# Kernel tuning notes

Measured on AMD Instinct MI355X. Metric: run time of the kernel, lower is better.

The kernel has to match this reference:

```python
import jax, jax.numpy as jnp
import numpy as np

N, C, D, V, NC = 60000, 4, 200, 5000, 250


def _lin(key, out_d, in_d):
    # torch nn.Linear default init: U(-1/sqrt(in), 1/sqrt(in))
    s = 1.0 / np.sqrt(in_d)
    k1, k2 = jax.random.split(key)
    w = jax.random.uniform(k1, (out_d, in_d), minval=-s, maxval=s, dtype=jnp.float32)
    b = jax.random.uniform(k2, (out_d,), minval=-s, maxval=s, dtype=jnp.float32)
    return w, b


def setup_inputs() -> dict:
    key = jax.random.key(0)
    ks = jax.random.split(key, 16)
    inp = {}
    inp['tokens'] = jax.random.randint(ks[0], (N,), 0, V)
    inp['child_c'] = jax.random.normal(ks[1], (N, C, D), dtype=jnp.float32)
    inp['child_h'] = jax.random.normal(ks[2], (N, C, D), dtype=jnp.float32)
    inp['emb'] = jax.random.normal(ks[3], (V, D), dtype=jnp.float32)
    # ForBlock: proj1: 3D->D, proj2: 2D->D
    inp['p1_w'], inp['p1_b'] = _lin(ks[4], D, 3 * D)
    inp['p2_w'], inp['p2_b'] = _lin(ks[5], D, 2 * D)
    # treelstm gates (each Linear D->D)
    for i, g in enumerate(['ix', 'ih', 'fx', 'fh', 'ux', 'uh', 'ox', 'oh']):
        w, b = _lin(ks[6 + i], D, D)
        inp[g + '_w'], inp[g + '_b'] = w, b
    inp['fc2_w'], inp['fc2_b'] = _lin(ks[14], NC, D)
    return inp


def reference(tokens, child_c, child_h, emb,
              p1_w, p1_b, p2_w, p2_b,
              ix_w, ix_b, ih_w, ih_b, fx_w, fx_b, fh_w, fh_b,
              ux_w, ux_b, uh_w, uh_b, ox_w, ox_b, oh_w, oh_b,
              fc2_w, fc2_b):
    x = emb[tokens]  # [N, D] node token embeddings (nn.Embedding lookup)
    # ForBlock: control = relu(proj1(cat[init, cond, next])); hsum = relu(proj2(cat[control, block]))
    control = jax.nn.relu(
        jnp.concatenate([child_h[:, 0], child_h[:, 1], child_h[:, 2]], axis=-1) @ p1_w.T + p1_b)
    child_h_sum = jax.nn.relu(
        jnp.concatenate([control, child_h[:, 3]], axis=-1) @ p2_w.T + p2_b)  # [N, D]
    # treelstm.node update (vectorized over N nodes, C children)
    i = jax.nn.sigmoid(x @ ix_w.T + ix_b + child_h_sum @ ih_w.T + ih_b)
    o = jax.nn.sigmoid(x @ ox_w.T + ox_b + child_h_sum @ oh_w.T + oh_b)
    u = jnp.tanh(x @ ux_w.T + ux_b + child_h_sum @ uh_w.T + uh_b)
    fx = (x @ fx_w.T + fx_b)[:, None, :]  # [N, 1, D]
    f = jax.nn.sigmoid(jnp.einsum('ncd,md->ncm', child_h, fh_w) + fh_b + fx)  # [N, C, D]
    c = i * u + jnp.sum(f * child_c, axis=1)  # [N, D]
    h = o * jnp.tanh(c)  # [N, D]
    logits = h @ fc2_w.T + fc2_b  # [N, n_class]
    return logits
```

## Files before the change

### kernel.cpp

```cpp
#include <hip/hip_runtime.h>
#include <cmath>

#define NNODES 60000
#define DDIM   200
#define NCLS   250

constexpr int R   = 32;
constexpr int BK  = 32;
constexpr int XP  = 208;

constexpr int O_X  = 0;
constexpr int O_H  = R * XP;
constexpr int O_A  = 2 * R * XP;
constexpr int AS   = R * BK;
constexpr int O_W  = O_A + 2 * AS;
constexpr int WS   = 8192;
constexpr int SH_TOT = O_W + 2 * WS + 32;

typedef float  f32x4  __attribute__((ext_vector_type(4)));
typedef short  short8 __attribute__((ext_vector_type(8)));

constexpr int W_P1  = 0;
constexpr int W_P2A = 155648;
constexpr int W_P2B = 212992;
constexpr int W_FX  = 270336;
constexpr int W_FH  = 327680;
constexpr int W_IX  = 385024;
constexpr int W_IH  = 442368;
constexpr int W_UX  = 499712;
constexpr int W_UH  = 557056;
constexpr int W_OX  = 614400;
constexpr int W_OH  = 671744;
constexpr int W_FC2 = 729088;
constexpr int W_TOTAL_ELEMS = 786432;
constexpr size_t W_TOTAL_BYTES = (size_t)W_TOTAL_ELEMS * 2;

__device__ __forceinline__ short f2b(float f) {
    union { float f; unsigned u; } x; x.f = f;
    unsigned r = (x.u + 0x7FFFu + ((x.u >> 16) & 1u)) >> 16;
    return (short)r;
}
__device__ __forceinline__ unsigned cvtpk(float lo, float hi) {
    unsigned r; asm("v_cvt_pk_bf16_f32 %0, %1, %2" : "=v"(r) : "v"(lo), "v"(hi));
    return r;
}
__device__ __forceinline__ short f2b1(float f) { return (short)(cvtpk(f, f) & 0xffffu); }
__device__ __forceinline__ float b2f(short s) {
    union { unsigned u; float f; } x; x.u = ((unsigned)(unsigned short)s) << 16;
    return x.f;
}
__device__ __forceinline__ float b2f_lo(unsigned u) { return b2f((short)(u & 0xffffu)); }
__device__ __forceinline__ float b2f_hi(unsigned u) { return b2f((short)(u >> 16)); }
__device__ __forceinline__ float sgm(float x)  { return 1.0f / (1.0f + __expf(-x)); }
__device__ __forceinline__ float tanh_fast(float x) { return 1.0f - 2.0f / (__expf(2.0f * x) + 1.0f); }
__device__ __forceinline__ int   swz(int b)    { return b ^ (((b >> 7) & 3) << 4); }
__device__ __forceinline__ short8 cvt8(float4 f0, float4 f1) {
    union { unsigned u[4]; short8 s; } c;
    c.u[0] = cvtpk(f0.x, f0.y); c.u[1] = cvtpk(f0.z, f0.w);
    c.u[2] = cvtpk(f1.x, f1.y); c.u[3] = cvtpk(f1.z, f1.w);
    return c.s;
}

__global__ void wprep(const float* __restrict__ p1w, const float* __restrict__ p2w,
                      const float* __restrict__ fxw, const float* __restrict__ fhw,
                      const float* __restrict__ ixw, const float* __restrict__ ihw,
                      const float* __restrict__ uxw, const float* __restrict__ uhw,
                      const float* __restrict__ oxw, const float* __restrict__ ohw,
                      const float* __restrict__ fc2w, short* __restrict__ ws)
{
    int i = blockIdx.x * 256 + threadIdx.x;
    if (i >= W_TOTAL_ELEMS) return;
    float v = 0.0f;
    if (i < W_P2A) {
        int n = i / 608, k = i % 608;
        if (n < 200 && k < 600) v = p1w[n * 600 + k];
        ws[i] = f2b(v); return;
    }
    int j = i - W_P2A;
    int m = j / 57344, rem = j % 57344;
    int n = rem / 224, k = rem % 224;
    const float* src; int stride = 200, off = 0, ncols = 200;
    switch (m) {
        case 0:  src = p2w; stride = 400; break;
        case 1:  src = p2w; stride = 400; off = 200; break;
        case 2:  src = fxw; break;
        case 3:  src = fhw; break;
        case 4:  src = ixw; break;
        case 5:  src = ihw; break;
        case 6:  src = uxw; break;
        case 7:  src = uhw; break;
        case 8:  src = oxw; break;
        case 9:  src = ohw; break;
        default: src = fc2w; ncols = 250; break;
    }
    if (n < ncols && k < 200) v = src[n * stride + off + k];
    ws[i] = f2b(v);
}

__device__ __forceinline__ void gload16(const void* g, void* l) {
    __builtin_amdgcn_global_load_lds((const __attribute__((address_space(1))) unsigned*)g,
                                     (__attribute__((address_space(3))) unsigned*)l, 16, 0, 0);
}

__device__ __forceinline__ void stage_w(const short* __restrict__ wmat, int Kpad, int t,
                                        int wrows, int wv, short* w_sw)
{
    const int issues = wrows >> 4;
    for (int q = wv; q < issues; q += 4) {
        const int lane = threadIdx.x & 63;
        const int db = q * 1024 + lane * 16;
        const int n  = db >> 6;
        const int g  = (db >> 4) & 3;
        const int gs = g ^ ((n >> 1) & 3);
        const short* src = wmat + (long)n * Kpad + t * BK + gs * 8;
        char* dst = ((char*)w_sw) + q * 1024;
        gload16(src, dst);
    }
}

__device__ __forceinline__ void stage_a_chh(short* a_sw, const float* __restrict__ ag,
                                            int row0, int colofs, int k0, int Kreal, int tid)
{
    if (tid >= 4 * R) return;
    const int r = tid >> 2, gq = tid & 3;
    const float* src = ag + (long)(row0 + r) * 800 + colofs + k0 + gq * 8;
    short8 v;
    if (k0 + BK <= Kreal) {
        float4 f0 = *(const float4*)(src);
        float4 f1 = *(const float4*)(src + 4);
        v = cvt8(f0, f1);
    } else {
        #pragma unroll
        for (int i = 0; i < 8; ++i) {
            int k = k0 + gq * 8 + i;
            float f = (k < Kreal) ? src[i] : 0.0f;
            v[i] = f2b(f);
        }
    }
    int b = r * 64 + gq * 16; b = swz(b);
    *(short8*)((char*)a_sw + b) = v;
}

template<int NF, bool FROM_GLOBAL>
__device__ __forceinline__ void gemm_pass(
    f32x4 (&acc)[NF],
    const short* __restrict__ Ap,
    const float* __restrict__ ag, int row0, int colofs, int Kreal,
    const short* __restrict__ wmat, int ktiles, int Kpad, int wrows,
    short* a_sw, short* w_sw,
    int tid, int wv, int wm, int wn, int l15, int lg)
{
    stage_w(wmat, Kpad, 0, wrows, wv, w_sw);
    if constexpr (FROM_GLOBAL)
        stage_a_chh(a_sw, ag, row0, colofs, 0, Kreal, tid);
    asm volatile("s_waitcnt vmcnt(0) lgkmcnt(0)" ::: "memory");
    __builtin_amdgcn_s_barrier();
    for (int t = 0; t < ktiles; ++t) {
        const int cur = t & 1, nxt = cur ^ 1;
        if (t + 1 < ktiles) {
            stage_w(wmat, Kpad, t + 1, wrows, wv, w_sw + nxt * WS);
            if constexpr (FROM_GLOBAL)
                stage_a_chh(a_sw + nxt * AS, ag, row0, colofs, (t + 1) * BK, Kreal, tid);
        }
        short8 af;
        const int row = wm * 16 + l15;
        if constexpr (FROM_GLOBAL)
            af = *(const short8*)((const char*)(a_sw + cur * AS) + swz(row * 64 + lg * 16));
        else
            af = *(const short8*)(Ap + row * XP + t * BK + lg * 8);
        #pragma unroll
        for (int ni = 0; ni < NF; ++ni) {
            const int n = (wn * NF + ni) * 16 + l15;
            short8 bf = *(const short8*)((const char*)(w_sw + cur * WS) + swz(n * 64 + lg * 16));
            acc[ni] = __builtin_amdgcn_mfma_f32_16x16x32_bf16(af, bf, acc[ni], 0, 0, 0);
        }
        asm volatile("s_waitcnt vmcnt(0) lgkmcnt(0)" ::: "memory");
        __builtin_amdgcn_s_barrier();
    }
}

#define Z7(A)  { _Pragma("unroll") for (int z_=0; z_<7; ++z_) { _Pragma("unroll") for (int q_=0;q_<4;++q_) A[z_][q_] = 0.0f; } }
#define Z8(A)  { _Pragma("unroll") for (int z_=0; z_<8; ++z_) { _Pragma("unroll") for (int q_=0;q_<4;++q_) A[z_][q_] = 0.0f; } }

__global__ __launch_bounds__(256, 2)
void fused_v7(const int* __restrict__ tok,
              const float* __restrict__ chc,
              const float* __restrict__ chh,
              const float* __restrict__ emb,
              const float* __restrict__ p1b_, const float* __restrict__ p2b_,
              const float* __restrict__ ixb, const float* __restrict__ ihb,
              const float* __restrict__ fxb, const float* __restrict__ fhb,
              const float* __restrict__ uxb, const float* __restrict__ uhb,
              const float* __restrict__ oxb, const float* __restrict__ ohb,
              const float* __restrict__ fc2b,
              const short* __restrict__ ws,
              float* __restrict__ out)
{
    __shared__ __align__(16) short SH[SH_TOT];
    short* X    = SH + O_X;
    short* H    = SH + O_H;
    short* a_sw = SH + O_A;
    short* w_sw = SH + O_W;

    const int tid = threadIdx.x;
    const int wv = tid >> 6, wm = wv >> 1, wn = wv & 1;
    const int l15 = tid & 15, lg = (tid & 63) >> 4;
    const int row0 = blockIdx.x * R;

    {
        short8 z = (short8)0;
        short8* shv = (short8*)SH;
        #pragma unroll 1
        for (int i = tid; i < SH_TOT / 8; i += 256) shv[i] = z;
    }
    __syncthreads();
    {
        #pragma unroll
        for (int it = 0; it < 4; ++it) {
            int u = tid + it * 256;
            if (u < 800) {
                int r = u / 25, cu = (u % 25) * 8;
                const float* s = emb + (long)tok[row0 + r] * DDIM + cu;
                float4 f0 = *(const float4*)s, f1 = *(const float4*)(s + 4);
                *(short8*)(X + r * XP + cu) = cvt8(f0, f1);
            }
        }
    }
    __syncthreads();

    f32x4 g[7];

    unsigned fxr[7][2];
    Z7(g);
    gemm_pass<7, false>(g, X, nullptr, 0, 0, 0, ws + W_FX, 7, 224, 224,
                        a_sw, w_sw, tid, wv, wm, wn, l15, lg);
    #pragma unroll
    for (int ni = 0; ni < 7; ++ni) {
        const int col = (wn * 7 + ni) * 16 + l15;
        const float b = (col < DDIM) ? fxb[col] : 0.0f;
        fxr[ni][0] = cvtpk(g[ni][0] + b, g[ni][1] + b);
        fxr[ni][1] = cvtpk(g[ni][2] + b, g[ni][3] + b);
    }

    float csum[7][4];
    #pragma unroll
    for (int ni = 0; ni < 7; ++ni)
        #pragma unroll
        for (int j = 0; j < 4; ++j) csum[ni][j] = 0.0f;

    #pragma unroll 1
    for (int c = 0; c < 4; ++c) {
        Z7(g);
        gemm_pass<7, true>(g, nullptr, chh, row0, c * 200, 200, ws + W_FH, 7, 224, 224,
                           a_sw, w_sw, tid, wv, wm, wn, l15, lg);
        #pragma unroll
        for (int ni = 0; ni < 7; ++ni) {
            const int col = (wn * 7 + ni) * 16 + l15;
            if (col < DDIM) {
                const float fb = fhb[col];
                #pragma unroll
                for (int j = 0; j < 4; ++j) {
                    const int lr = wm * 16 + lg * 4 + j;
                    const float cv = chc[(long)(row0 + lr) * 800 + c * 200 + col];
                    const unsigned pk = fxr[ni][j >> 1];
                    const float fx = (j & 1) ? b2f_hi(pk) : b2f_lo(pk);
                    csum[ni][j] += sgm(g[ni][j] + fb + fx) * cv;
                }
            }
        }
    }

    Z7(g);
    gemm_pass<7, true>(g, nullptr, chh, row0, 0, 600, ws + W_P1, 19, 608, 224,
                       a_sw, w_sw, tid, wv, wm, wn, l15, lg);
    #pragma unroll
    for (int ni = 0; ni < 7; ++ni) {
        const int col = (wn * 7 + ni) * 16 + l15;
        if (col < DDIM) {
            const float b = p1b_[col];
            #pragma unroll
            for (int j = 0; j < 4; ++j) {
                const int lr = wm * 16 + lg * 4 + j;
                H[lr * XP + col] = f2b1(fmaxf(g[ni][j] + b, 0.0f));
            }
        }
    }
    __syncthreads();

    Z7(g);
    gemm_pass<7, false>(g, H, nullptr, 0, 0, 0, ws + W_P2A, 7, 224, 224,
                        a_sw, w_sw, tid, wv, wm, wn, l15, lg);
    gemm_pass<7, true>(g, nullptr, chh, row0, 600, 200, ws + W_P2B, 7, 224, 224,
                       a_sw, w_sw, tid, wv, wm, wn, l15, lg);
    #pragma unroll
    for (int ni = 0; ni < 7; ++ni) {
        const int col = (wn * 7 + ni) * 16 + l15;
        if (col < DDIM) {
            const float b = p2b_[col];
            #pragma unroll
            for (int j = 0; j < 4; ++j) {
                const int lr = wm * 16 + lg * 4 + j;
                H[lr * XP + col] = f2b1(fmaxf(g[ni][j] + b, 0.0f));
            }
        }
    }
    __syncthreads();

    unsigned gi[7][2];
    Z7(g);
    gemm_pass<7, false>(g, X, nullptr, 0, 0, 0, ws + W_IX, 7, 224, 224,
                        a_sw, w_sw, tid, wv, wm, wn, l15, lg);
    gemm_pass<7, false>(g, H, nullptr, 0, 0, 0, ws + W_IH, 7, 224, 224,
                        a_sw, w_sw, tid, wv, wm, wn, l15, lg);
    #pragma unroll
    for (int ni = 0; ni < 7; ++ni) {
        const int col = (wn * 7 + ni) * 16 + l15;
        const float b = (col < DDIM) ? (ixb[col] + ihb[col]) : 0.0f;
        gi[ni][0] = cvtpk(sgm(g[ni][0] + b), sgm(g[ni][1] + b));
        gi[ni][1] = cvtpk(sgm(g[ni][2] + b), sgm(g[ni][3] + b));
    }

    Z7(g);
    gemm_pass<7, false>(g, X, nullptr, 0, 0, 0, ws + W_UX, 7, 224, 224,
                        a_sw, w_sw, tid, wv, wm, wn, l15, lg);
    gemm_pass<7, false>(g, H, nullptr, 0, 0, 0, ws + W_UH, 7, 224, 224,
                        a_sw, w_sw, tid, wv, wm, wn, l15, lg);
    #pragma unroll
    for (int ni = 0; ni < 7; ++ni) {
        const int col = (wn * 7 + ni) * 16 + l15;
        const float b = (col < DDIM) ? (uxb[col] + uhb[col]) : 0.0f;
        #pragma unroll
        for (int j = 0; j < 4; ++j) {
            const unsigned pk = gi[ni][j >> 1];
            const float iv = (j & 1) ? b2f_hi(pk) : b2f_lo(pk);
            csum[ni][j] = iv * tanh_fast(g[ni][j] + b) + csum[ni][j];
        }
    }

    Z7(g);
    gemm_pass<7, false>(g, X, nullptr, 0, 0, 0, ws + W_OX, 7, 224, 224,
                        a_sw, w_sw, tid, wv, wm, wn, l15, lg);
    gemm_pass<7, false>(g, H, nullptr, 0, 0, 0, ws + W_OH, 7, 224, 224,
                        a_sw, w_sw, tid, wv, wm, wn, l15, lg);
    #pragma unroll
    for (int ni = 0; ni < 7; ++ni) {
        const int col = (wn * 7 + ni) * 16 + l15;
        if (col < DDIM) {
            const float b = oxb[col] + ohb[col];
            #pragma unroll
            for (int j = 0; j < 4; ++j) {
                const int lr = wm * 16 + lg * 4 + j;
                H[lr * XP + col] = f2b1(sgm(g[ni][j] + b) * tanh_fast(csum[ni][j]));
            }
        }
    }
    __syncthreads();

    f32x4 o8[8];
    Z8(o8);
    gemm_pass<8, false>(o8, H, nullptr, 0, 0, 0, ws + W_FC2, 7, 224, 256,
                        a_sw, w_sw, tid, wv, wm, wn, l15, lg);
    #pragma unroll
    for (int ni = 0; ni < 8; ++ni) {
        const int col = (wn * 8 + ni) * 16 + l15;
        if (col < NCLS) {
            const float b = fc2b[col];
            #pragma unroll
            for (int j = 0; j < 4; ++j) {
                const int lr = wm * 16 + lg * 4 + j;
                out[(long)(row0 + lr) * NCLS + col] = o8[ni][j] + b;
            }
        }
    }
}

constexpr int FRT = 32, FBK = 16, FNT = 256, FRTP = FRT + 4, FBUFP = 208;
__device__ __forceinline__ float sgm_f(float x) { return 1.0f / (1.0f + expf(-x)); }

__device__ __forceinline__ void f_stage(
    float (*aT)[FRTP], float (*wt)[FNT], int row0, int k0,
    const float* a1g, int a1pitch, const int* gidx, const float* a1l, int a1lp, int K1,
    const float* a2g, int a2pitch, const float* a2l, int a2lp, int K2,
    const float* wa, int wap, int KW1, const float* wb, int wbp,
    int ncols, int tid)
{
    const int Ktot = K1 + K2;
    {
        const int kk = tid & 15, k = k0 + kk;
        #pragma unroll
        for (int h = 0; h < 2; ++h) {
            const int r = (tid >> 4) + h * 16;
            float v = 0.0f;
            if (k < K1) {
                if (a1l) v = a1l[r * a1lp + k];
                else {
                    const long rb = gidx ? (long)gidx[row0 + r] * a1pitch : (long)(row0 + r) * a1pitch;
                    v = a1g[rb + k];
                }
            } else if (k < Ktot) {
                if (a2l) v = a2l[r * a2lp + (k - K1)];
                else     v = a2g[(long)(row0 + r) * a2pitch + (k - K1)];
            }
            aT[kk][r] = v;
        }
    }
    {
        const int col = tid;
        #pragma unroll
        for (int kk = 0; kk < FBK; ++kk) {
            const int k = k0 + kk; float v = 0.0f;
            if (col < ncols && k < Ktot) {
                if (k < KW1) v = wa[(long)col * wap + k];
                else         v = wb[(long)col * wbp + (k - KW1)];
            }
            wt[kk][col] = v;
        }
    }
}
__device__ __forceinline__ void f_gemm(
    float (*aT)[FRTP], float (*wt)[FNT], float acc[8][4], int row0,
    const float* a1g, int a1p, const int* gidx, const float* a1l, int a1lp, int K1,
    const float* a2g, int a2p, const float* a2l, int a2lp, int K2,
    const float* wa, int wap, int KW1, const float* wb, int wbp,
    int ncols, int tid, int tr, int tc)
{
    #pragma unroll
    for (int j = 0; j < 8; ++j)
        #pragma unroll
        for (int i = 0; i < 4; ++i) acc[j][i] = 0.0f;
    const int Ktot = K1 + K2;
    for (int k0 = 0; k0 < Ktot; k0 += FBK) {
        __syncthreads();
        f_stage(aT, wt, row0, k0, a1g, a1p, gidx, a1l, a1lp, K1, a2g, a2p, a2l, a2lp, K2,
                wa, wap, KW1, wb, wbp, ncols, tid);
        __syncthreads();
        #pragma unroll
        for (int kk = 0; kk < FBK; ++kk) {
            const float w0 = wt[kk][tc*4+0], w1 = wt[kk][tc*4+1], w2 = wt[kk][tc*4+2], w3 = wt[kk][tc*4+3];
            #pragma unroll
            for (int j = 0; j < 8; ++j) {
                const float a = aT[kk][tr*8+j];
                acc[j][0] = fmaf(a, w0, acc[j][0]); acc[j][1] = fmaf(a, w1, acc[j][1]);
                acc[j][2] = fmaf(a, w2, acc[j][2]); acc[j][3] = fmaf(a, w3, acc[j][3]);
            }
        }
    }
}
__global__ __launch_bounds__(256)
void fused_fp32(const int* tok, const float* chc, const float* chh, const float* emb,
                const float* p1w, const float* p1b, const float* p2w, const float* p2b,
                const float* ixw, const float* ixb, const float* ihw, const float* ihb,
                const float* fxw, const float* fxb, const float* fhw, const float* fhb,
                const float* uxw, const float* uxb, const float* uhw, const float* uhb,
                const float* oxw, const float* oxb, const float* ohw, const float* ohb,
                const float* fc2w, const float* fc2b, float* out)
{
    __shared__ float aT[FBK][FRTP]; __shared__ float wt[FBK][FNT]; __shared__ float buf[FRT][FBUFP];
    const int tid = threadIdx.x, tr = tid >> 6, tc = tid & 63, c0 = tc * 4;
    const int row0 = blockIdx.x * FRT;
    float acc[8][4];
    f_gemm(aT, wt, acc, row0, chh, 800, nullptr, nullptr, 0, 600, nullptr,0,nullptr,0,0, p1w,600,600,nullptr,0, DDIM, tid,tr,tc);
    if (c0 < DDIM) { const float4 b = *(const float4*)&p1b[c0];
        #pragma unroll
        for (int j=0;j<8;++j){int r=tr*8+j; buf[r][c0]=fmaxf(acc[j][0]+b.x,0.f); buf[r][c0+1]=fmaxf(acc[j][1]+b.y,0.f); buf[r][c0+2]=fmaxf(acc[j][2]+b.z,0.f); buf[r][c0+3]=fmaxf(acc[j][3]+b.w,0.f);} }
    f_gemm(aT, wt, acc, row0, nullptr,0,nullptr,&buf[0][0],FBUFP,200, chh+600,800,nullptr,0,200, p2w,400,400,nullptr,0, DDIM, tid,tr,tc);
    if (c0 < DDIM) { const float4 b = *(const float4*)&p2b[c0];
        #pragma unroll
        for (int j=0;j<8;++j){int r=tr*8+j; buf[r][c0]=fmaxf(acc[j][0]+b.x,0.f); buf[r][c0+1]=fmaxf(acc[j][1]+b.y,0.f); buf[r][c0+2]=fmaxf(acc[j][2]+b.z,0.f); buf[r][c0+3]=fmaxf(acc[j][3]+b.w,0.f);} }
    f_gemm(aT, wt, acc, row0, emb, DDIM, tok, nullptr,0,200, nullptr,0,nullptr,0,0, fxw,200,200,nullptr,0, DDIM, tid,tr,tc);
    float fxr[8][4];
    { float4 b = make_float4(0,0,0,0); if (c0<DDIM) b = *(const float4*)&fxb[c0];
      #pragma unroll
      for (int j=0;j<8;++j){fxr[j][0]=acc[j][0]+b.x;fxr[j][1]=acc[j][1]+b.y;fxr[j][2]=acc[j][2]+b.z;fxr[j][3]=acc[j][3]+b.w;} }
    float csum[8][4];
    #pragma unroll
    for (int j=0;j<8;++j)
        #pragma unroll
        for (int i=0;i<4;++i) csum[j][i]=0.f;
    for (int cc_=0; cc_<4; ++cc_) {
        f_gemm(aT, wt, acc, row0, chh+cc_*200,800,nullptr,nullptr,0,200, nullptr,0,nullptr,0,0, fhw,200,200,nullptr,0, DDIM, tid,tr,tc);
        if (c0 < DDIM) { const float4 b = *(const float4*)&fhb[c0];
            #pragma unroll
            for (int j=0;j<8;++j){ const long r=row0+tr*8+j; const float4 cv=*(const float4*)&chc[r*800+cc_*200+c0];
                csum[j][0]+=sgm_f(acc[j][0]+b.x+fxr[j][0])*cv.x; csum[j][1]+=sgm_f(acc[j][1]+b.y+fxr[j][1])*cv.y;
                csum[j][2]+=sgm_f(acc[j][2]+b.z+fxr[j][2])*cv.z; csum[j][3]+=sgm_f(acc[j][3]+b.w+fxr[j][3])*cv.w; } }
    }
    f_gemm(aT, wt, acc, row0, emb, DDIM, tok, nullptr,0,200, nullptr,0,&buf[0][0],FBUFP,200, ixw,200,200,ihw,200, DDIM, tid,tr,tc);
    float gi[8][4];
    { float4 b1=make_float4(0,0,0,0),b2=b1; if(c0<DDIM){b1=*(const float4*)&ixb[c0];b2=*(const float4*)&ihb[c0];}
      #pragma unroll
      for(int j=0;j<8;++j){gi[j][0]=sgm_f(acc[j][0]+b1.x+b2.x);gi[j][1]=sgm_f(acc[j][1]+b1.y+b2.y);gi[j][2]=sgm_f(acc[j][2]+b1.z+b2.z);gi[j][3]=sgm_f(acc[j][3]+b1.w+b2.w);} }
    f_gemm(aT, wt, acc, row0, emb, DDIM, tok, nullptr,0,200, nullptr,0,&buf[0][0],FBUFP,200, uxw,200,200,uhw,200, DDIM, tid,tr,tc);
    float cval[8][4];
    { float4 b1=make_float4(0,0,0,0),b2=b1; if(c0<DDIM){b1=*(const float4*)&uxb[c0];b2=*(const float4*)&uhb[c0];}
      #pragma unroll
      for(int j=0;j<8;++j){cval[j][0]=gi[j][0]*tanhf(acc[j][0]+b1.x+b2.x)+csum[j][0];cval[j][1]=gi[j][1]*tanhf(acc[j][1]+b1.y+b2.y)+csum[j][1];
                           cval[j][2]=gi[j][2]*tanhf(acc[j][2]+b1.z+b2.z)+csum[j][2];cval[j][3]=gi[j][3]*tanhf(acc[j][3]+b1.w+b2.w)+csum[j][3];} }
    f_gemm(aT, wt, acc, row0, emb, DDIM, tok, nullptr,0,200, nullptr,0,&buf[0][0],FBUFP,200, oxw,200,200,ohw,200, DDIM, tid,tr,tc);
    if (c0 < DDIM) { const float4 b1=*(const float4*)&oxb[c0], b2=*(const float4*)&ohb[c0];
        #pragma unroll
        for(int j=0;j<8;++j){int r=tr*8+j;
            buf[r][c0]=sgm_f(acc[j][0]+b1.x+b2.x)*tanhf(cval[j][0]); buf[r][c0+1]=sgm_f(acc[j][1]+b1.y+b2.y)*tanhf(cval[j][1]);
            buf[r][c0+2]=sgm_f(acc[j][2]+b1.z+b2.z)*tanhf(cval[j][2]); buf[r][c0+3]=sgm_f(acc[j][3]+b1.w+b2.w)*tanhf(cval[j][3]);} }
    f_gemm(aT, wt, acc, row0, nullptr,0,nullptr,&buf[0][0],FBUFP,200, nullptr,0,nullptr,0,0, fc2w,200,200,nullptr,0, NCLS, tid,tr,tc);
    #pragma unroll
    for (int j=0;j<8;++j){ const long r=row0+tr*8+j;
        #pragma unroll
        for (int i=0;i<4;++i){ const int col=c0+i; if (col<NCLS) out[r*NCLS+col]=acc[j][i]+fc2b[col]; } }
}

extern "C" void kernel_launch(void* const* d_in, const int* in_sizes, int n_in,
                              void* d_out, int out_size, void* d_ws, size_t ws_size,
                              hipStream_t stream)
{
    const int*   tok  = (const int*)  d_in[0];
    const float* chc  = (const float*)d_in[1];
    const float* chh  = (const float*)d_in[2];
    const float* emb  = (const float*)d_in[3];
    const float* p1w  = (const float*)d_in[4];
    const float* p1b  = (const float*)d_in[5];
    const float* p2w  = (const float*)d_in[6];
    const float* p2b  = (const float*)d_in[7];
    const float* ixw  = (const float*)d_in[8];
    const float* ixb  = (const float*)d_in[9];
    const float* ihw  = (const float*)d_in[10];
    const float* ihb  = (const float*)d_in[11];
    const float* fxw  = (const float*)d_in[12];
    const float* fxb  = (const float*)d_in[13];
    const float* fhw  = (const float*)d_in[14];
    const float* fhb  = (const float*)d_in[15];
    const float* uxw  = (const float*)d_in[16];
    const float* uxb  = (const float*)d_in[17];
    const float* uhw  = (const float*)d_in[18];
    const float* uhb  = (const float*)d_in[19];
    const float* oxw  = (const float*)d_in[20];
    const float* oxb  = (const float*)d_in[21];
    const float* ohw  = (const float*)d_in[22];
    const float* ohb  = (const float*)d_in[23];
    const float* fc2w = (const float*)d_in[24];
    const float* fc2b = (const float*)d_in[25];
    float* out = (float*)d_out;

    if (ws_size >= W_TOTAL_BYTES) {
        short* ws = (short*)d_ws;
        hipLaunchKernelGGL(wprep, dim3((W_TOTAL_ELEMS + 255) / 256), dim3(256), 0, stream,
                           p1w, p2w, fxw, fhw, ixw, ihw, uxw, uhw, oxw, ohw, fc2w, ws);
        hipLaunchKernelGGL(fused_v7, dim3(NNODES / R), dim3(256), 0, stream,
                           tok, chc, chh, emb,
                           p1b, p2b, ixb, ihb, fxb, fhb, uxb, uhb, oxb, ohb, fc2b,
                           ws, out);
    } else {
        hipLaunchKernelGGL(fused_fp32, dim3(NNODES / FRT), dim3(256), 0, stream,
                           tok, chc, chh, emb, p1w, p1b, p2w, p2b,
                           ixw, ixb, ihw, ihb, fxw, fxb, fhw, fhb,
                           uxw, uxb, uhw, uhb, oxw, oxb, ohw, ohb, fc2w, fc2b, out);
    }
}
```

Before: 449.8 us.

## Double row tile to 64 with 512-thread blocks and restage gate epilogues

Each block now handles 64 rows with 8 waves arranged 2x4, and each wave computes two M sub-tiles against four N sub-tiles, so every staged weight tile feeds twice as many MFMAs. The stage order changes: proj1/proj2 run first, then the i/u/o gates, whose results are kept packed in registers, then the forget-gate loop, which builds the cell state directly. Padding is changed to XP=232 and bounds clamps are added because 60000 is not a multiple of 64. The goal is to cut repeated weight staging and barrier overhead per row. The cost is roughly 100KB of LDS per block, which allows only one block per CU, plus higher register pressure.

Result: slower. 492.1 us (+9.4%).

```diff
diff --git a/kernel.cpp b/kernel.cpp
--- a/kernel.cpp
+++ b/kernel.cpp
@@ -5,9 +5,9 @@
 #define DDIM   200
 #define NCLS   250
 
-constexpr int R   = 32;
+constexpr int R   = 64;
 constexpr int BK  = 32;
-constexpr int XP  = 208;
+constexpr int XP  = 232;
 
 constexpr int O_X  = 0;
 constexpr int O_H  = R * XP;
@@ -106,7 +106,7 @@
                                         int wrows, int wv, short* w_sw)
 {
     const int issues = wrows >> 4;
-    for (int q = wv; q < issues; q += 4) {
+    for (int q = wv; q < issues; q += 8) {
         const int lane = threadIdx.x & 63;
         const int db = q * 1024 + lane * 16;
         const int n  = db >> 6;
@@ -123,7 +123,8 @@
 {
     if (tid >= 4 * R) return;
     const int r = tid >> 2, gq = tid & 3;
-    const float* src = ag + (long)(row0 + r) * 800 + colofs + k0 + gq * 8;
+    long rg = row0 + r; if (rg >= NNODES) rg = NNODES - 1;
+    const float* src = ag + rg * 800 + colofs + k0 + gq * 8;
     short8 v;
     if (k0 + BK <= Kreal) {
         float4 f0 = *(const float4*)(src);
@@ -143,7 +144,7 @@
 
 template<int NF, bool FROM_GLOBAL>
 __device__ __forceinline__ void gemm_pass(
-    f32x4 (&acc)[NF],
+    f32x4 (&acc)[2][NF],
     const short* __restrict__ Ap,
     const float* __restrict__ ag, int row0, int colofs, int Kreal,
     const short* __restrict__ wmat, int ktiles, int Kpad, int wrows,
@@ -153,8 +154,7 @@
     stage_w(wmat, Kpad, 0, wrows, wv, w_sw);
     if constexpr (FROM_GLOBAL)
         stage_a_chh(a_sw, ag, row0, colofs, 0, Kreal, tid);
-    asm volatile("s_waitcnt vmcnt(0) lgkmcnt(0)" ::: "memory");
-    __builtin_amdgcn_s_barrier();
+    __syncthreads();
     for (int t = 0; t < ktiles; ++t) {
         const int cur = t & 1, nxt = cur ^ 1;
         if (t + 1 < ktiles) {
@@ -162,28 +162,30 @@
             if constexpr (FROM_GLOBAL)
                 stage_a_chh(a_sw + nxt * AS, ag, row0, colofs, (t + 1) * BK, Kreal, tid);
         }
-        short8 af;
-        const int row = wm * 16 + l15;
-        if constexpr (FROM_GLOBAL)
-            af = *(const short8*)((const char*)(a_sw + cur * AS) + swz(row * 64 + lg * 16));
-        else
-            af = *(const short8*)(Ap + row * XP + t * BK + lg * 8);
+        short8 af[2];
+        #pragma unroll
+        for (int mi = 0; mi < 2; ++mi) {
+            const int row = wm * 32 + mi * 16 + l15;
+            if constexpr (FROM_GLOBAL)
+                af[mi] = *(const short8*)((const char*)(a_sw + cur * AS) + swz(row * 64 + lg * 16));
+            else
+                af[mi] = *(const short8*)(Ap + row * XP + t * BK + lg * 8);
+        }
         #pragma unroll
         for (int ni = 0; ni < NF; ++ni) {
             const int n = (wn * NF + ni) * 16 + l15;
             short8 bf = *(const short8*)((const char*)(w_sw + cur * WS) + swz(n * 64 + lg * 16));
-            acc[ni] = __builtin_amdgcn_mfma_f32_16x16x32_bf16(af, bf, acc[ni], 0, 0, 0);
-        }
-        asm volatile("s_waitcnt vmcnt(0) lgkmcnt(0)" ::: "memory");
-        __builtin_amdgcn_s_barrier();
-    }
-}
-
-#define Z7(A)  { _Pragma("unroll") for (int z_=0; z_<7; ++z_) { _Pragma("unroll") for (int q_=0;q_<4;++q_) A[z_][q_] = 0.0f; } }
-#define Z8(A)  { _Pragma("unroll") for (int z_=0; z_<8; ++z_) { _Pragma("unroll") for (int q_=0;q_<4;++q_) A[z_][q_] = 0.0f; } }
-
-__global__ __launch_bounds__(256, 2)
-void fused_v7(const int* __restrict__ tok,
+            acc[0][ni] = __builtin_amdgcn_mfma_f32_16x16x32_bf16(af[0], bf, acc[0][ni], 0, 0, 0);
+            acc[1][ni] = __builtin_amdgcn_mfma_f32_16x16x32_bf16(af[1], bf, acc[1][ni], 0, 0, 0);
+        }
+        __syncthreads();
+    }
+}
+
+#define Z24(A)  { _Pragma("unroll") for (int m_=0;m_<2;++m_) { _Pragma("unroll") for (int z_=0; z_<4; ++z_) { _Pragma("unroll") for (int q_=0;q_<4;++q_) A[m_][z_][q_] = 0.0f; } } }
+
+__global__ __launch_bounds__(512, 1)
+void fused_v8(const int* __restrict__ tok,
               const float* __restrict__ chc,
               const float* __restrict__ chh,
               const float* __restrict__ emb,
@@ -203,7 +205,9 @@
     short* w_sw = SH + O_W;
 
     const int tid = threadIdx.x;
-    const int wv = tid >> 6, wm = wv >> 1, wn = wv & 1;
+    const int wv  = tid >> 6;
+    const int wm  = wv >> 2;
+    const int wn  = wv & 3;
     const int l15 = tid & 15, lg = (tid & 63) >> 4;
     const int row0 = blockIdx.x * R;
 
@@ -211,167 +215,195 @@
         short8 z = (short8)0;
         short8* shv = (short8*)SH;
         #pragma unroll 1
-        for (int i = tid; i < SH_TOT / 8; i += 256) shv[i] = z;
+        for (int i = tid; i < SH_TOT / 8; i += 512) shv[i] = z;
     }
     __syncthreads();
     {
-        #pragma unroll
-        for (int it = 0; it < 4; ++it) {
-            int u = tid + it * 256;
-            if (u < 800) {
-                int r = u / 25, cu = (u % 25) * 8;
-                const float* s = emb + (long)tok[row0 + r] * DDIM + cu;
-                float4 f0 = *(const float4*)s, f1 = *(const float4*)(s + 4);
-                *(short8*)(X + r * XP + cu) = cvt8(f0, f1);
-            }
+        #pragma unroll 1
+        for (int u = tid; u < 1600; u += 512) {
+            int r = u / 25, cu = (u % 25) * 8;
+            long rg = row0 + r; if (rg >= NNODES) rg = NNODES - 1;
+            const float* s = emb + (long)tok[rg] * DDIM + cu;
+            float4 f0 = *(const float4*)s, f1 = *(const float4*)(s + 4);
+            *(short8*)(X + r * XP + cu) = cvt8(f0, f1);
         }
     }
     __syncthreads();
 
-    f32x4 g[7];
-
-    unsigned fxr[7][2];
-    Z7(g);
-    gemm_pass<7, false>(g, X, nullptr, 0, 0, 0, ws + W_FX, 7, 224, 224,
-                        a_sw, w_sw, tid, wv, wm, wn, l15, lg);
-    #pragma unroll
-    for (int ni = 0; ni < 7; ++ni) {
-        const int col = (wn * 7 + ni) * 16 + l15;
-        const float b = (col < DDIM) ? fxb[col] : 0.0f;
-        fxr[ni][0] = cvtpk(g[ni][0] + b, g[ni][1] + b);
-        fxr[ni][1] = cvtpk(g[ni][2] + b, g[ni][3] + b);
-    }
-
-    float csum[7][4];
-    #pragma unroll
-    for (int ni = 0; ni < 7; ++ni)
-        #pragma unroll
-        for (int j = 0; j < 4; ++j) csum[ni][j] = 0.0f;
+    f32x4 g[2][4];
+
+    Z24(g);
+    gemm_pass<4, true>(g, nullptr, chh, row0, 0, 600, ws + W_P1, 19, 608, 224,
+                       a_sw, w_sw, tid, wv, wm, wn, l15, lg);
+    #pragma unroll
+    for (int mi = 0; mi < 2; ++mi)
+        #pragma unroll
+        for (int ni = 0; ni < 4; ++ni) {
+            const int col = (wn * 4 + ni) * 16 + l15;
+            if (col < DDIM) {
+                const float b = p1b_[col];
+                #pragma unroll
+                for (int j = 0; j < 4; ++j) {
+                    const int lr = wm * 32 + mi * 16 + lg * 4 + j;
+                    H[lr * XP + col] = f2b1(fmaxf(g[mi][ni][j] + b, 0.0f));
+                }
+            }
+        }
+
+    Z24(g);
+    gemm_pass<4, false>(g, H, nullptr, 0, 0, 0, ws + W_P2A, 7, 224, 224,
+                        a_sw, w_sw, tid, wv, wm, wn, l15, lg);
+    gemm_pass<4, true>(g, nullptr, chh, row0, 600, 200, ws + W_P2B, 7, 224, 224,
+                       a_sw, w_sw, tid, wv, wm, wn, l15, lg);
+    #pragma unroll
+    for (int mi = 0; mi < 2; ++mi)
+        #pragma unroll
+        for (int ni = 0; ni < 4; ++ni) {
+            const int col = (wn * 4 + ni) * 16 + l15;
+            if (col < DDIM) {
+                const float b = p2b_[col];
+                #pragma unroll
+                for (int j = 0; j < 4; ++j) {
+                    const int lr = wm * 32 + mi * 16 + lg * 4 + j;
+                    H[lr * XP + col] = f2b1(fmaxf(g[mi][ni][j] + b, 0.0f));
+                }
+            }
+        }
+
+    unsigned gi[2][4][2];
+    Z24(g);
+    gemm_pass<4, false>(g, X, nullptr, 0, 0, 0, ws + W_IX, 7, 224, 224,
+                        a_sw, w_sw, tid, wv, wm, wn, l15, lg);
+    gemm_pass<4, false>(g, H, nullptr, 0, 0, 0, ws + W_IH, 7, 224, 224,
+                        a_sw, w_sw, tid, wv, wm, wn, l15, lg);
+    #pragma unroll
+    for (int mi = 0; mi < 2; ++mi)
+        #pragma unroll
+        for (int ni = 0; ni < 4; ++ni) {
+            const int col = (wn * 4 + ni) * 16 + l15;
+            const float b = (col < DDIM) ? (ixb[col] + ihb[col]) : 0.0f;
+            gi[mi][ni][0] = cvtpk(sgm(g[mi][ni][0] + b), sgm(g[mi][ni][1] + b));
+            gi[mi][ni][1] = cvtpk(sgm(g[mi][ni][2] + b), sgm(g[mi][ni][3] + b));
+        }
+
+    unsigned iu[2][4][2];
+    Z24(g);
+    gemm_pass<4, false>(g, X, nullptr, 0, 0, 0, ws + W_UX, 7, 224, 224,
+                        a_sw, w_sw, tid, wv, wm, wn, l15, lg);
+    gemm_pass<4, false>(g, H, nullptr, 0, 0, 0, ws + W_UH, 7, 224, 224,
+                        a_sw, w_sw, tid, wv, wm, wn, l15, lg);
+    #pragma unroll
+    for (int mi = 0; mi < 2; ++mi)
+        #pragma unroll
+        for (int ni = 0; ni < 4; ++ni) {
+            const int col = (wn * 4 + ni) * 16 + l15;
+            const float b = (col < DDIM) ? (uxb[col] + uhb[col]) : 0.0f;
+            float v0 = b2f_lo(gi[mi][ni][0]) * tanh_fast(g[mi][ni][0] + b);
+            float v1 = b2f_hi(gi[mi][ni][0]) * tanh_fast(g[mi][ni][1] + b);
+            float v2 = b2f_lo(gi[mi][ni][1]) * tanh_fast(g[mi][ni][2] + b);
+            float v3 = b2f_hi(gi[mi][ni][1]) * tanh_fast(g[mi][ni][3] + b);
+            iu[mi][ni][0] = cvtpk(v0, v1);
+            iu[mi][ni][1] = cvtpk(v2, v3);
+        }
+
+    unsigned og[2][4][2];
+    Z24(g);
+    gemm_pass<4, false>(g, X, nullptr, 0, 0, 0, ws + W_OX, 7, 224, 224,
+                        a_sw, w_sw, tid, wv, wm, wn, l15, lg);
+    gemm_pass<4, false>(g, H, nullptr, 0, 0, 0, ws + W_OH, 7, 224, 224,
+                        a_sw, w_sw, tid, wv, wm, wn, l15, lg);
+    #pragma unroll
+    for (int mi = 0; mi < 2; ++mi)
+        #pragma unroll
+        for (int ni = 0; ni < 4; ++ni) {
+            const int col = (wn * 4 + ni) * 16 + l15;
+            const float b = (col < DDIM) ? (oxb[col] + ohb[col]) : 0.0f;
+            og[mi][ni][0] = cvtpk(sgm(g[mi][ni][0] + b), sgm(g[mi][ni][1] + b));
+            og[mi][ni][1] = cvtpk(sgm(g[mi][ni][2] + b), sgm(g[mi][ni][3] + b));
+        }
+
+    unsigned fxr[2][4][2];
+    Z24(g);
+    gemm_pass<4, false>(g, X, nullptr, 0, 0, 0, ws + W_FX, 7, 224, 224,
+                        a_sw, w_sw, tid, wv, wm, wn, l15, lg);
+    #pragma unroll
+    for (int mi = 0; mi < 2; ++mi)
+        #pragma unroll
+        for (int ni = 0; ni < 4; ++ni) {
+            const int col = (wn * 4 + ni) * 16 + l15;
+            const float b = (col < DDIM) ? fxb[col] : 0.0f;
+            fxr[mi][ni][0] = cvtpk(g[mi][ni][0] + b, g[mi][ni][1] + b);
+            fxr[mi][ni][1] = cvtpk(g[mi][ni][2] + b, g[mi][ni][3] + b);
+        }
+
+    float csum[2][4][4];
+    #pragma unroll
+    for (int mi = 0; mi < 2; ++mi)
+        #pragma unroll
+        for (int ni = 0; ni < 4; ++ni)
+            #pragma unroll
+            for (int j = 0; j < 4; ++j) csum[mi][ni][j] = 0.0f;
 
     #pragma unroll 1
     for (int c = 0; c < 4; ++c) {
-        Z7(g);
-        gemm_pass<7, true>(g, nullptr, chh, row0, c * 200, 200, ws + W_FH, 7, 224, 224,
+        Z24(g);
+        gemm_pass<4, true>(g, nullptr, chh, row0, c * 200, 200, ws + W_FH, 7, 224, 224,
                            a_sw, w_sw, tid, wv, wm, wn, l15, lg);
         #pragma unroll
-        for (int ni = 0; ni < 7; ++ni) {
-            const int col = (wn * 7 + ni) * 16 + l15;
+        for (int mi = 0; mi < 2; ++mi)
+            #pragma unroll
+            for (int ni = 0; ni < 4; ++ni) {
+                const int col = (wn * 4 + ni) * 16 + l15;
+                if (col < DDIM) {
+                    const float fb = fhb[col];
+                    #pragma unroll
+                    for (int j = 0; j < 4; ++j) {
+                        long rg = row0 + wm * 32 + mi * 16 + lg * 4 + j;
+                        if (rg >= NNODES) rg = NNODES - 1;
+                        const float cv = chc[rg * 800 + c * 200 + col];
+                        const unsigned pk = fxr[mi][ni][j >> 1];
+                        const float fx = (j & 1) ? b2f_hi(pk) : b2f_lo(pk);
+                        csum[mi][ni][j] += sgm(g[mi][ni][j] + fb + fx) * cv;
+                    }
+                }
+            }
+    }
+
+    #pragma unroll
+    for (int mi = 0; mi < 2; ++mi)
+        #pragma unroll
+        for (int ni = 0; ni < 4; ++ni) {
+            const int col = (wn * 4 + ni) * 16 + l15;
             if (col < DDIM) {
-                const float fb = fhb[col];
                 #pragma unroll
                 for (int j = 0; j < 4; ++j) {
-                    const int lr = wm * 16 + lg * 4 + j;
-                    const float cv = chc[(long)(row0 + lr) * 800 + c * 200 + col];
-                    const unsigned pk = fxr[ni][j >> 1];
-                    const float fx = (j & 1) ? b2f_hi(pk) : b2f_lo(pk);
-                    csum[ni][j] += sgm(g[ni][j] + fb + fx) * cv;
+                    const int lr = wm * 32 + mi * 16 + lg * 4 + j;
+                    const unsigned pi = iu[mi][ni][j >> 1];
+                    const unsigned po = og[mi][ni][j >> 1];
+                    const float iv = (j & 1) ? b2f_hi(pi) : b2f_lo(pi);
+                    const float ov = (j & 1) ? b2f_hi(po) : b2f_lo(po);
+                    H[lr * XP + col] = f2b1(ov * tanh_fast(iv + csum[mi][ni][j]));
                 }
             }
         }
-    }
-
-    Z7(g);
-    gemm_pass<7, true>(g, nullptr, chh, row0, 0, 600, ws + W_P1, 19, 608, 224,
-                       a_sw, w_sw, tid, wv, wm, wn, l15, lg);
-    #pragma unroll
-    for (int ni = 0; ni < 7; ++ni) {
-        const int col = (wn * 7 + ni) * 16 + l15;
-        if (col < DDIM) {
-            const float b = p1b_[col];
-            #pragma unroll
-            for (int j = 0; j < 4; ++j) {
-                const int lr = wm * 16 + lg * 4 + j;
-                H[lr * XP + col] = f2b1(fmaxf(g[ni][j] + b, 0.0f));
-            }
-        }
-    }
-    __syncthreads();
-
-    Z7(g);
-    gemm_pass<7, false>(g, H, nullptr, 0, 0, 0, ws + W_P2A, 7, 224, 224,
-                        a_sw, w_sw, tid, wv, wm, wn, l15, lg);
-    gemm_pass<7, true>(g, nullptr, chh, row0, 600, 200, ws + W_P2B, 7, 224, 224,
-                       a_sw, w_sw, tid, wv, wm, wn, l15, lg);
-    #pragma unroll
-    for (int ni = 0; ni < 7; ++ni) {
-        const int col = (wn * 7 + ni) * 16 + l15;
-        if (col < DDIM) {
-            const float b = p2b_[col];
-            #pragma unroll
-            for (int j = 0; j < 4; ++j) {
-                const int lr = wm * 16 + lg * 4 + j;
-                H[lr * XP + col] = f2b1(fmaxf(g[ni][j] + b, 0.0f));
-            }
-        }
-    }
-    __syncthreads();
-
-    unsigned gi[7][2];
-    Z7(g);
-    gemm_pass<7, false>(g, X, nullptr, 0, 0, 0, ws + W_IX, 7, 224, 224,
-                        a_sw, w_sw, tid, wv, wm, wn, l15, lg);
-    gemm_pass<7, false>(g, H, nullptr, 0, 0, 0, ws + W_IH, 7, 224, 224,
-                        a_sw, w_sw, tid, wv, wm, wn, l15, lg);
-    #pragma unroll
-    for (int ni = 0; ni < 7; ++ni) {
-        const int col = (wn * 7 + ni) * 16 + l15;
-        const float b = (col < DDIM) ? (ixb[col] + ihb[col]) : 0.0f;
-        gi[ni][0] = cvtpk(sgm(g[ni][0] + b), sgm(g[ni][1] + b));
-        gi[ni][1] = cvtpk(sgm(g[ni][2] + b), sgm(g[ni][3] + b));
-    }
-
-    Z7(g);
-    gemm_pass<7, false>(g, X, nullptr, 0, 0, 0, ws + W_UX, 7, 224, 224,
-                        a_sw, w_sw, tid, wv, wm, wn, l15, lg);
-    gemm_pass<7, false>(g, H, nullptr, 0, 0, 0, ws + W_UH, 7, 224, 224,
-                        a_sw, w_sw, tid, wv, wm, wn, l15, lg);
-    #pragma unroll
-    for (int ni = 0; ni < 7; ++ni) {
-        const int col = (wn * 7 + ni) * 16 + l15;
-        const float b = (col < DDIM) ? (uxb[col] + uhb[col]) : 0.0f;
-        #pragma unroll
-        for (int j = 0; j < 4; ++j) {
-            const unsigned pk = gi[ni][j >> 1];
-            const float iv = (j & 1) ? b2f_hi(pk) : b2f_lo(pk);
-            csum[ni][j] = iv * tanh_fast(g[ni][j] + b) + csum[ni][j];
-        }
-    }
-
-    Z7(g);
-    gemm_pass<7, false>(g, X, nullptr, 0, 0, 0, ws + W_OX, 7, 224, 224,
-                        a_sw, w_sw, tid, wv, wm, wn, l15, lg);
-    gemm_pass<7, false>(g, H, nullptr, 0, 0, 0, ws + W_OH, 7, 224, 224,
-                        a_sw, w_sw, tid, wv, wm, wn, l15, lg);
-    #pragma unroll
-    for (int ni = 0; ni < 7; ++ni) {
-        const int col = (wn * 7 + ni) * 16 + l15;
-        if (col < DDIM) {
-            const float b = oxb[col] + ohb[col];
-            #pragma unroll
-            for (int j = 0; j < 4; ++j) {
-                const int lr = wm * 16 + lg * 4 + j;
-                H[lr * XP + col] = f2b1(sgm(g[ni][j] + b) * tanh_fast(csum[ni][j]));
-            }
-        }
-    }
-    __syncthreads();
-
-    f32x4 o8[8];
-    Z8(o8);
-    gemm_pass<8, false>(o8, H, nullptr, 0, 0, 0, ws + W_FC2, 7, 224, 256,
-                        a_sw, w_sw, tid, wv, wm, wn, l15, lg);
-    #pragma unroll
-    for (int ni = 0; ni < 8; ++ni) {
-        const int col = (wn * 8 + ni) * 16 + l15;
-        if (col < NCLS) {
-            const float b = fc2b[col];
-            #pragma unroll
-            for (int j = 0; j < 4; ++j) {
-                const int lr = wm * 16 + lg * 4 + j;
-                out[(long)(row0 + lr) * NCLS + col] = o8[ni][j] + b;
-            }
-        }
-    }
+
+    Z24(g);
+    gemm_pass<4, false>(g, H, nullptr, 0, 0, 0, ws + W_FC2, 7, 224, 256,
+                        a_sw, w_sw, tid, wv, wm, wn, l15, lg);
+    #pragma unroll
+    for (int mi = 0; mi < 2; ++mi)
+        #pragma unroll
+        for (int ni = 0; ni < 4; ++ni) {
+            const int col = (wn * 4 + ni) * 16 + l15;
+            if (col < NCLS) {
+                const float b = fc2b[col];
+                #pragma unroll
+                for (int j = 0; j < 4; ++j) {
+                    const long gr = row0 + wm * 32 + mi * 16 + lg * 4 + j;
+                    if (gr < NNODES) out[gr * NCLS + col] = g[mi][ni][j] + b;
+                }
+            }
+        }
 }
 
 constexpr int FRT = 32, FBK = 16, FNT = 256, FRTP = FRT + 4, FBUFP = 208;
@@ -545,7 +577,7 @@
         short* ws = (short*)d_ws;
         hipLaunchKernelGGL(wprep, dim3((W_TOTAL_ELEMS + 255) / 256), dim3(256), 0, stream,
                            p1w, p2w, fxw, fhw, ixw, ihw, uxw, uhw, oxw, ohw, fc2w, ws);
-        hipLaunchKernelGGL(fused_v7, dim3(NNODES / R), dim3(256), 0, stream,
+        hipLaunchKernelGGL(fused_v8, dim3((NNODES + R - 1) / R), dim3(512), 0, stream,
                            tok, chc, chh, emb,
                            p1b, p2b, ixb, ihb, fxb, fhb, uxb, uhb, oxb, ohb, fc2b,
                            ws, out);
```
